# Optimization experiments

Measured on AMD Instinct MI355X. Metric: run time of the kernel, lower is better.

The kernel has to match this reference:

```python
import jax, jax.numpy as jnp
import numpy as np

B, T, K, V, D, C = 16, 16, 4, 10003, 256, 64  # batch, traj_len, beam, lid_size+3, dim_embed_loc, dim_com


def setup_inputs() -> dict:
    key = jax.random.key(0)
    ks = jax.random.split(key, 9)
    return {
        "loc_tar": jax.random.randint(ks[0], (B, T), 0, V),
        "zs": jax.random.normal(ks[1], (B, D), jnp.float32),
        "zt": jax.random.normal(ks[2], (B, D), jnp.float32),
        "E": jax.random.normal(ks[3], (V, D), jnp.float32) * 0.02,    # loc embedding table
        "W_v": jax.random.normal(ks[4], (D, V), jnp.float32) * 0.02,  # decoder output proj
        "b_v": jnp.zeros((V,), jnp.float32),
        "W_c": jax.random.normal(ks[5], (D, C), jnp.float32) * 0.05,  # LocCompressor
        "b_c": jnp.zeros((C,), jnp.float32),
        "W_t": jax.random.normal(ks[6], (C,), jnp.float32) * 0.05,    # temporal decoder
        "W_zt": jax.random.normal(ks[7], (D,), jnp.float32) * 0.05,
    }


def _decode(loc_tar, zs, E, W_v, b_v):
    # Beam-search decode faithful to the torch inference branch:
    # per-step full-seq decoder fwd, log_softmax, topk, (log-prob) product,
    # descending sort over M*K candidates, gather top 2K chains.
    chain_r = loc_tar.at[:, 1:].set(0)   # [B,T]; keep BOS, zero rest
    zs_r = zs                            # [B,D]
    prob = None
    for i in range(T - 1):
        emb = E[chain_r]                                     # [N,T,D] gather
        h = emb + zs_r[:, None, :]
        logp = jax.nn.log_softmax(h @ W_v + b_v, axis=-1)    # [N,T,V]
        p_i, idx_i = jax.lax.top_k(logp[:, i, :], K)         # [N,K]
        if i == 0:
            chain_r = jnp.repeat(chain_r, K, axis=0).at[:, 1].set(idx_i.reshape(-1))  # [B*K,T]
            prob = p_i                                       # [B,K]
            zs_r = jnp.repeat(zs_r, K, axis=0)
        else:
            M = chain_r.shape[0] // B                        # K at i=1, 2K after
            # NOTE: original multiplies log-probs (faithful to source)
            prob2 = (prob[:, :, None] * p_i.reshape(B, M, K)).reshape(B, M * K)
            order = jnp.argsort(-prob2, axis=-1)             # descending sort
            prob = jnp.take_along_axis(prob2, order, axis=-1)[:, :2 * K]
            ch = jnp.repeat(chain_r, K, axis=0).at[:, i + 1].set(idx_i.reshape(-1))
            ch = ch.reshape(B, M * K, T)
            chain_r = ch[jnp.arange(B)[:, None], order[:, :2 * K]].reshape(-1, T)  # [B*2K,T]
            zs_r = jnp.repeat(zs, 2 * K, axis=0)
    return chain_r.reshape(B, -1, T)[:, 0, 1:-1]             # best beam, [B,T-2]


def reference(loc_tar, zs, zt, E, W_v, b_v, W_c, b_c, W_t, W_zt):
    loc_chain = _decode(loc_tar, zs, E, W_v, b_v)            # [B,T-2] int
    loc_info = jnp.tanh(E[loc_chain] @ W_c + b_c)            # LocCompressor, [B,T-2,C]
    tim_chain = loc_info @ W_t + (zt @ W_zt)[:, None]        # temporal decoder, [B,T-2]
    return loc_chain, tim_chain
```

## Files before the change

### kernel.cpp

```cpp
#include <hip/hip_runtime.h>
#include <math.h>

#define BB 16
#define TT 16
#define KK 4
#define VV 10003
#define DD 256
#define CC 64
#define RPB 4
#define VT  1280
#define NVT 8
#define VP 10016
#define FNEG (-1e30f)

typedef float f32x4 __attribute__((ext_vector_type(4)));
typedef float f32x4u __attribute__((ext_vector_type(4), aligned(4)));

struct L4 { float v0, v1, v2, v3; int i0, i1, i2, i3; };

__device__ __forceinline__ void l4_init(L4 &l) {
  l.v0 = l.v1 = l.v2 = l.v3 = FNEG;
  l.i0 = l.i1 = l.i2 = l.i3 = 0x7fffffff;
}
__device__ __forceinline__ bool better(float v, int ix, float v2, int ix2) {
  return (v > v2) || (v == v2 && ix < ix2);
}
__device__ __forceinline__ void l4_insert(L4 &l, float v, int ix) {
  const bool c0 = better(v, ix, l.v0, l.i0);
  const bool c1 = better(v, ix, l.v1, l.i1);
  const bool c2 = better(v, ix, l.v2, l.i2);
  const bool c3 = better(v, ix, l.v3, l.i3);
  l.v3 = c3 ? (c2 ? l.v2 : v) : l.v3;  l.i3 = c3 ? (c2 ? l.i2 : ix) : l.i3;
  l.v2 = c2 ? (c1 ? l.v1 : v) : l.v2;  l.i2 = c2 ? (c1 ? l.i1 : ix) : l.i2;
  l.v1 = c1 ? (c0 ? l.v0 : v) : l.v1;  l.i1 = c1 ? (c0 ? l.i0 : ix) : l.i1;
  l.v0 = c0 ? v : l.v0;                l.i0 = c0 ? ix : l.i0;
}
__device__ __forceinline__ void l4_merge(L4 &a, const L4 &b) {
  l4_insert(a, b.v0, b.i0);
  l4_insert(a, b.v1, b.i1);
  l4_insert(a, b.v2, b.i2);
  l4_insert(a, b.v3, b.i3);
}
__device__ __forceinline__ L4 l4_shfl_xor(const L4 &a, int off) {
  L4 o;
  o.v0 = __shfl_xor(a.v0, off); o.i0 = __shfl_xor(a.i0, off);
  o.v1 = __shfl_xor(a.v1, off); o.i1 = __shfl_xor(a.i1, off);
  o.v2 = __shfl_xor(a.v2, off); o.i2 = __shfl_xor(a.i2, off);
  o.v3 = __shfl_xor(a.v3, off); o.i3 = __shfl_xor(a.i3, off);
  return o;
}

__global__ __launch_bounds__(256, 1)
void k_gemm(const float* __restrict__ E, const float* __restrict__ zs,
            const float* __restrict__ Wv, const float* __restrict__ bv,
            const int* __restrict__ loc_tar,
            const float* __restrict__ topP, const int* __restrict__ topI,
            const float* __restrict__ probIn, const int* __restrict__ chainIn,
            float* __restrict__ probOut, int* __restrict__ chainOut,
            float* __restrict__ Lg, int step, int N, int Mshift) {
  __shared__ __align__(16) float xs[RPB * DD];
  __shared__ int cs[RPB];
  __shared__ int selSrc[BB][8];
  __shared__ int selTok[BB][8];
  __shared__ float prS[BB * 8];

  const int t = threadIdx.x;
  const int tile = blockIdx.x % NVT;
  const int n0 = (blockIdx.x / NVT) * RPB;
  const int v0 = tile * VT;

  const int v4 = v0 + (t << 2);
  const int v1 = v0 + 1024 + t;
  const int v1ok = (v1 < VV);
  const int v1c = v1ok ? v1 : (VV - 1);

  if (step >= 2) {
    const int M = (step == 2) ? 4 : 8;
    const int nc = M * 4;
    const int c = t & 31;
    const int bh = t >> 5;
    for (int h = 0; h < 2; ++h) {
      const int b = bh + h * 8;
      float act;
      if (c < nc) {
        int mi = c >> 2, k = c & 3;
        act = probIn[b * 8 + mi] * topP[(b * M + mi) * 4 + k];
      } else {
        act = -INFINITY;
      }
      for (int j = 0; j < 8; ++j) {
        float rv = act; int ri = c;
#pragma unroll
        for (int off = 1; off < 32; off <<= 1) {
          float v2 = __shfl_xor(rv, off, 32);
          int   i2 = __shfl_xor(ri, off, 32);
          if (v2 > rv || (v2 == rv && i2 < ri)) { rv = v2; ri = i2; }
        }
        if (c == ri) act = -INFINITY;
        if (c == 0) {
          int mi = ri >> 2, k = ri & 3;
          int src = b * M + mi;
          int tok = topI[src * 4 + k]; if ((unsigned)tok >= VV) tok = 0;
          selSrc[b][j] = src;
          selTok[b][j] = tok;
          prS[b * 8 + j] = rv;
        }
      }
    }
    __syncthreads();
  }

  if (t < RPB) {
    int n = n0 + t;
    int ctok;
    if (step == 0)      ctok = loc_tar[n * TT];
    else if (step == 1) ctok = topI[(n >> 2) * 4 + (n & 3)];
    else                ctok = selTok[n >> 3][n & 7];
    if ((unsigned)ctok >= VV) ctok = 0;
    cs[t] = ctok;
  }
  __syncthreads();

  if (blockIdx.x == 0 && step >= 1) {
    if (step == 1) {
      for (int e = t; e < BB * KK * TT; e += 256) {
        int dst = e >> 4, q = e & 15;
        int bb = dst >> 2, kk = dst & 3;
        int val;
        if (q == 1) { int tok = topI[bb * 4 + kk]; if ((unsigned)tok >= VV) tok = 0; val = tok; }
        else if (q == 0) val = loc_tar[bb * TT];
        else val = 0;
        chainOut[dst * TT + q] = val;
      }
      if (t < BB * KK) {
        int bb = t >> 2, kk = t & 3;
        probOut[bb * 8 + kk] = topP[bb * 4 + kk];
      }
    } else {
      for (int e = t; e < BB * 8 * TT; e += 256) {
        int dst = e >> 4, q = e & 15;
        int bb = dst >> 3, j = dst & 7;
        int src = selSrc[bb][j];
        int val = (q == step) ? selTok[bb][j] : chainIn[src * TT + q];
        chainOut[dst * TT + q] = val;
      }
      if (t < BB * 8) probOut[t] = prS[t];
    }
  }

  for (int e = t; e < RPB * DD; e += 256) {
    int r = e >> 8, d = e & 255;
    int n = n0 + r;
    int b = n >> Mshift;
    xs[e] = E[cs[r] * DD + d] + zs[b * DD + d];
  }
  __syncthreads();

  const float* w4p = Wv + v4;
  const float* w1p = Wv + v1c;

  float acc4[RPB][4];
  float acc1[RPB];
#pragma unroll
  for (int r = 0; r < RPB; ++r) {
    acc1[r] = 0.f;
#pragma unroll
    for (int j = 0; j < 4; ++j) acc4[r][j] = 0.f;
  }

  f32x4u w4A[8], w4B[8];
  float  w1A[8], w1B[8];
  f32x4  h0A[RPB], h1A[RPB], h0B[RPB], h1B[RPB];

#pragma unroll
  for (int u = 0; u < 8; ++u) {
    w4A[u] = *(const f32x4u*)(w4p + (size_t)u * VV);
    w1A[u] = w1p[(size_t)u * VV];
  }
#pragma unroll
  for (int r = 0; r < RPB; ++r) {
    h0A[r] = *(const f32x4*)(xs + r * DD);
    h1A[r] = *(const f32x4*)(xs + r * DD + 4);
  }

  for (int d0 = 0; d0 < DD; d0 += 16) {
    const int dB = d0 + 8;
#pragma unroll
    for (int u = 0; u < 8; ++u) {
      w4B[u] = *(const f32x4u*)(w4p + (size_t)(dB + u) * VV);
      w1B[u] = w1p[(size_t)(dB + u) * VV];
    }
#pragma unroll
    for (int r = 0; r < RPB; ++r) {
      h0B[r] = *(const f32x4*)(xs + r * DD + dB);
      h1B[r] = *(const f32x4*)(xs + r * DD + dB + 4);
    }

#pragma unroll
    for (int u = 0; u < 8; ++u) {
#pragma unroll
      for (int r = 0; r < RPB; ++r) {
        const float hv = (u < 4) ? h0A[r][u] : h1A[r][u - 4];
#pragma unroll
        for (int j = 0; j < 4; ++j) acc4[r][j] = fmaf(hv, w4A[u][j], acc4[r][j]);
        acc1[r] = fmaf(hv, w1A[u], acc1[r]);
      }
    }

    const int dA = (d0 + 16 < DD) ? (d0 + 16) : 0;
#pragma unroll
    for (int u = 0; u < 8; ++u) {
      w4A[u] = *(const f32x4u*)(w4p + (size_t)(dA + u) * VV);
      w1A[u] = w1p[(size_t)(dA + u) * VV];
    }
#pragma unroll
    for (int r = 0; r < RPB; ++r) {
      h0A[r] = *(const f32x4*)(xs + r * DD + dA);
      h1A[r] = *(const f32x4*)(xs + r * DD + dA + 4);
    }

#pragma unroll
    for (int u = 0; u < 8; ++u) {
#pragma unroll
      for (int r = 0; r < RPB; ++r) {
        const float hv = (u < 4) ? h0B[r][u] : h1B[r][u - 4];
#pragma unroll
        for (int j = 0; j < 4; ++j) acc4[r][j] = fmaf(hv, w4B[u][j], acc4[r][j]);
        acc1[r] = fmaf(hv, w1B[u], acc1[r]);
      }
    }
  }

  const f32x4u bv4 = *(const f32x4u*)(bv + v4);
#pragma unroll
  for (int r = 0; r < RPB; ++r) {
    f32x4 o;
#pragma unroll
    for (int j = 0; j < 4; ++j) o[j] = acc4[r][j] + bv4[j];
    *(f32x4*)(Lg + (size_t)(n0 + r) * VP + v4) = o;
  }
  if (v1ok) {
    const float bvv = bv[v1];
#pragma unroll
    for (int r = 0; r < RPB; ++r)
      Lg[(size_t)(n0 + r) * VP + v1] = acc1[r] + bvv;
  }
}

__global__ __launch_bounds__(1024)
void k_red(const float* __restrict__ Lg, float* __restrict__ topP,
           int* __restrict__ topI) {
  __shared__ __align__(16) float row[VV];
  __shared__ float wmax[16];
  __shared__ float wv4[16 * 4];
  __shared__ int   wi4[16 * 4];
  __shared__ float leafS[128];

  const int n = blockIdx.x;
  const int t = threadIdx.x;
  const int lane = t & 63;
  const int wid = t >> 6;
  const float* grow = Lg + (size_t)n * VP;

  const int va = t << 2;
  const int vb = 4096 + (t << 2);
  const int vc = 8192 + (t << 2);
  f32x4 xa = *(const f32x4*)(grow + va);
  f32x4 xb = *(const f32x4*)(grow + vb);
  f32x4 xc;
  const bool cfull = (vc + 3 < VV);
  if (cfull) {
    xc = *(const f32x4*)(grow + vc);
  } else {
#pragma unroll
    for (int j = 0; j < 4; ++j) xc[j] = (vc + j < VV) ? grow[vc + j] : FNEG;
  }

  float m = FNEG;
  L4 top; l4_init(top);
#pragma unroll
  for (int j = 0; j < 4; ++j) { float x = xa[j]; if (x > m) m = x; l4_insert(top, x, va + j); }
#pragma unroll
  for (int j = 0; j < 4; ++j) { float x = xb[j]; if (x > m) m = x; l4_insert(top, x, vb + j); }
#pragma unroll
  for (int j = 0; j < 4; ++j) {
    if (vc + j < VV) { float x = xc[j]; if (x > m) m = x; l4_insert(top, x, vc + j); }
  }

  for (int off = 32; off; off >>= 1) {
    float m2 = __shfl_xor(m, off);
    if (m2 > m) m = m2;
    L4 o = l4_shfl_xor(top, off);
    l4_merge(top, o);
  }
  if (lane == 0) {
    wmax[wid] = m;
    wv4[wid * 4 + 0] = top.v0; wi4[wid * 4 + 0] = top.i0;
    wv4[wid * 4 + 1] = top.v1; wi4[wid * 4 + 1] = top.i1;
    wv4[wid * 4 + 2] = top.v2; wi4[wid * 4 + 2] = top.i2;
    wv4[wid * 4 + 3] = top.v3; wi4[wid * 4 + 3] = top.i3;
  }
  __syncthreads();

  float mm = wmax[lane & 15];
#pragma unroll
  for (int off = 8; off; off >>= 1) {
    float m2 = __shfl_xor(mm, off);
    if (m2 > mm) mm = m2;
  }
  const float gm = mm;

  L4 aa; l4_init(aa);
  if (wid == 0) {
    const int g = lane & 15;
    aa.v0 = wv4[g * 4 + 0]; aa.i0 = wi4[g * 4 + 0];
    aa.v1 = wv4[g * 4 + 1]; aa.i1 = wi4[g * 4 + 1];
    aa.v2 = wv4[g * 4 + 2]; aa.i2 = wi4[g * 4 + 2];
    aa.v3 = wv4[g * 4 + 3]; aa.i3 = wi4[g * 4 + 3];
#pragma unroll
    for (int off = 8; off; off >>= 1) {
      L4 o = l4_shfl_xor(aa, off);
      l4_merge(aa, o);
    }
  }

  {
    f32x4 ea, eb;
#pragma unroll
    for (int j = 0; j < 4; ++j) ea[j] = (float)exp((double)(xa[j] - gm));
#pragma unroll
    for (int j = 0; j < 4; ++j) eb[j] = (float)exp((double)(xb[j] - gm));
    *(f32x4*)(row + va) = ea;
    *(f32x4*)(row + vb) = eb;
    if (cfull) {
      f32x4 ec;
#pragma unroll
      for (int j = 0; j < 4; ++j) ec[j] = (float)exp((double)(xc[j] - gm));
      *(f32x4*)(row + vc) = ec;
    } else {
#pragma unroll
      for (int j = 0; j < 4; ++j)
        if (vc + j < VV) row[vc + j] = (float)exp((double)(xc[j] - gm));
    }
  }
  __syncthreads();

  {
    const int g = t >> 3, j = t & 7;
    int base = 0, nn = VV;
#pragma unroll
    for (int k = 6; k >= 0; --k) {
      int half = nn >> 1;
      int n2 = half - (half & 7);
      if ((g >> k) & 1) { base += n2; nn -= n2; } else nn = n2;
    }
    const float* a = row + base;
    const int full = nn & ~7;
    float r = a[j];
    for (int i = 8 + j; i < full; i += 8) r += a[i];
    float s = r + __shfl_xor(r, 1);
    s = s + __shfl_xor(s, 2);
    s = s + __shfl_xor(s, 4);
    if (j == 0) {
      for (int i = full; i < nn; ++i) s += a[i];
      leafS[g] = s;
    }
  }
  __syncthreads();

  if (t < 64) {
    float v = leafS[2 * t] + leafS[2 * t + 1];
#pragma unroll
    for (int l = 0; l < 6; ++l) {
      float x0 = __shfl(v, t * 2);
      float x1 = __shfl(v, t * 2 + 1);
      v = x0 + x1;
    }
    if (t == 0) {
      float ls = (float)log((double)v);
      topP[n * 4 + 0] = (aa.v0 - gm) - ls;  topI[n * 4 + 0] = aa.i0;
      topP[n * 4 + 1] = (aa.v1 - gm) - ls;  topI[n * 4 + 1] = aa.i1;
      topP[n * 4 + 2] = (aa.v2 - gm) - ls;  topI[n * 4 + 2] = aa.i2;
      topP[n * 4 + 3] = (aa.v3 - gm) - ls;  topI[n * 4 + 3] = aa.i3;
    }
  }
}

__global__ __launch_bounds__(64)
void k_final(const int* __restrict__ chainIn, const float* __restrict__ probIn,
             const float* __restrict__ topP, const int* __restrict__ topI,
             const float* __restrict__ E,
             const float* __restrict__ Wc, const float* __restrict__ bc,
             const float* __restrict__ Wt, const float* __restrict__ zt,
             const float* __restrict__ Wzt, float* __restrict__ out) {
  int blk = blockIdx.x;
  int b = blk / (TT - 2), tpos = blk % (TT - 2);
  int lane = threadIdx.x;

  const int c = lane & 31;
  int mi = c >> 2, k = c & 3;
  float act = probIn[b * 8 + mi] * topP[(b * 8 + mi) * 4 + k];
  float rv = act; int ri = c;
#pragma unroll
  for (int off = 1; off < 32; off <<= 1) {
    float v2 = __shfl_xor(rv, off, 32);
    int   i2 = __shfl_xor(ri, off, 32);
    if (v2 > rv || (v2 == rv && i2 < ri)) { rv = v2; ri = i2; }
  }
  const int src = b * 8 + (ri >> 2);
  int loc = chainIn[src * TT + 1 + tpos];
  if ((unsigned)loc >= VV) loc = 0;

  double acc = (double)bc[lane];
  const float* er = E + loc * DD;
  for (int d = 0; d < DD; ++d) acc += (double)er[d] * (double)Wc[d * CC + lane];
  double val = tanh(acc) * (double)Wt[lane];
  const float* ztr = zt + b * DD;
#pragma unroll
  for (int q = 0; q < 4; ++q) val += (double)ztr[lane * 4 + q] * (double)Wzt[lane * 4 + q];
  for (int off = 32; off; off >>= 1) val += __shfl_down(val, off);
  if (lane == 0) {
    out[b * (TT - 2) + tpos] = (float)loc;
    out[BB * (TT - 2) + b * (TT - 2) + tpos] = (float)val;
  }
}

extern "C" void kernel_launch(void* const* d_in, const int* in_sizes, int n_in,
                              void* d_out, int out_size, void* d_ws, size_t ws_size,
                              hipStream_t stream) {
  const int*   loc_tar = (const int*)  d_in[0];
  const float* zs      = (const float*)d_in[1];
  const float* zt      = (const float*)d_in[2];
  const float* E       = (const float*)d_in[3];
  const float* Wv      = (const float*)d_in[4];
  const float* bv      = (const float*)d_in[5];
  const float* Wc      = (const float*)d_in[6];
  const float* bc      = (const float*)d_in[7];
  const float* Wt      = (const float*)d_in[8];
  const float* Wzt     = (const float*)d_in[9];
  float* out = (float*)d_out;

  char* w = (char*)d_ws;
  float* Lg     = (float*)(w);
  float* topP   = (float*)(w + 5128192);
  int*   topI   = (int*)  (w + 5130240);
  float* probA  = (float*)(w + 5132288);
  float* probB  = (float*)(w + 5132800);
  int*   chainA = (int*)  (w + 5133312);
  int*   chainB = (int*)  (w + 5141504);

  float* pIn = probA; float* pOut = probB;
  int*   cIn = chainA; int*  cOut = chainB;

  k_gemm<<<(16 / RPB) * NVT, 256, 0, stream>>>(E, zs, Wv, bv, loc_tar,
      topP, topI, pIn, cIn, pOut, cOut, Lg, 0, 16, 0);
  k_red<<<16, 1024, 0, stream>>>(Lg, topP, topI);

  for (int i = 1; i < TT - 1; ++i) {
    int N = (i == 1) ? (BB * KK) : (BB * 2 * KK);
    int Mshift = (i == 1) ? 2 : 3;
    k_gemm<<<(N / RPB) * NVT, 256, 0, stream>>>(E, zs, Wv, bv, loc_tar,
        topP, topI, pIn, cIn, pOut, cOut, Lg, i, N, Mshift);
    k_red<<<N, 1024, 0, stream>>>(Lg, topP, topI);
    float* pt = pIn; pIn = pOut; pOut = pt;
    int*   ct = cIn; cIn = cOut; cOut = ct;
  }

  k_final<<<BB * (TT - 2), 64, 0, stream>>>(cIn, pIn, topP, topI,
                                            E, Wc, bc, Wt, zt, Wzt, out);
}
```

Baseline: 1.019 ms.

## Split vocab tiles finer, emit per-tile max from GEMM, split softmax reduction in halves

The GEMM now uses 16 vocab tiles of 640 columns with 2-wide vector loads and asks for two blocks per CU. Each block also writes per-row tile maxima, so the reduction kernel no longer computes the global max itself. The log-softmax/top-k reduction is split across two blocks per row, and a new small combine kernel merges the partial sums and top-4 lists. This raises parallelism at small batch sizes but adds one kernel launch per step and uses narrower loads per thread.

```diff
diff --git a/kernel.cpp b/kernel.cpp
--- a/kernel.cpp
+++ b/kernel.cpp
@@ -8,13 +8,15 @@
 #define DD 256
 #define CC 64
 #define RPB 4
-#define VT  1280
-#define NVT 8
+#define VT  640
+#define NVT 16
 #define VP 10016
 #define FNEG (-1e30f)
+#define NSPL 5000
 
 typedef float f32x4 __attribute__((ext_vector_type(4)));
 typedef float f32x4u __attribute__((ext_vector_type(4), aligned(4)));
+typedef float f32x2u __attribute__((ext_vector_type(2), aligned(4)));
 
 struct L4 { float v0, v1, v2, v3; int i0, i1, i2, i3; };
 
@@ -50,29 +52,34 @@
   return o;
 }
 
-__global__ __launch_bounds__(256, 1)
+__global__ __launch_bounds__(256, 2)
 void k_gemm(const float* __restrict__ E, const float* __restrict__ zs,
             const float* __restrict__ Wv, const float* __restrict__ bv,
             const int* __restrict__ loc_tar,
             const float* __restrict__ topP, const int* __restrict__ topI,
             const float* __restrict__ probIn, const int* __restrict__ chainIn,
             float* __restrict__ probOut, int* __restrict__ chainOut,
-            float* __restrict__ Lg, int step, int N, int Mshift) {
+            float* __restrict__ Lg, float* __restrict__ Gmax,
+            int step, int N, int Mshift) {
   __shared__ __align__(16) float xs[RPB * DD];
   __shared__ int cs[RPB];
   __shared__ int selSrc[BB][8];
   __shared__ int selTok[BB][8];
   __shared__ float prS[BB * 8];
+  __shared__ float wmx[4][RPB];
 
   const int t = threadIdx.x;
   const int tile = blockIdx.x % NVT;
   const int n0 = (blockIdx.x / NVT) * RPB;
   const int v0 = tile * VT;
 
-  const int v4 = v0 + (t << 2);
-  const int v1 = v0 + 1024 + t;
-  const int v1ok = (v1 < VV);
-  const int v1c = v1ok ? v1 : (VV - 1);
+  const int vp = v0 + (t << 1);
+  const int vpok = (vp + 1 < VV);
+  const int vpc = vpok ? vp : 0;
+  int ve = v0 + 512 + t;
+  int veok = (t < 128) && (ve < VV);
+  if (v0 + 512 >= VV && t == 0) { ve = VV - 1; veok = 1; }
+  const int vec = veok ? ve : (VV - 1);
 
   if (step >= 2) {
     const int M = (step == 2) ? 4 : 8;
@@ -156,25 +163,24 @@
   }
   __syncthreads();
 
-  const float* w4p = Wv + v4;
-  const float* w1p = Wv + v1c;
-
-  float acc4[RPB][4];
+  const float* w2p = Wv + vpc;
+  const float* w1p = Wv + vec;
+
+  float acc2[RPB][2];
   float acc1[RPB];
 #pragma unroll
   for (int r = 0; r < RPB; ++r) {
     acc1[r] = 0.f;
-#pragma unroll
-    for (int j = 0; j < 4; ++j) acc4[r][j] = 0.f;
-  }
-
-  f32x4u w4A[8], w4B[8];
+    acc2[r][0] = 0.f; acc2[r][1] = 0.f;
+  }
+
+  f32x2u w2A[8], w2B[8];
   float  w1A[8], w1B[8];
   f32x4  h0A[RPB], h1A[RPB], h0B[RPB], h1B[RPB];
 
 #pragma unroll
   for (int u = 0; u < 8; ++u) {
-    w4A[u] = *(const f32x4u*)(w4p + (size_t)u * VV);
+    w2A[u] = *(const f32x2u*)(w2p + (size_t)u * VV);
     w1A[u] = w1p[(size_t)u * VV];
   }
 #pragma unroll
@@ -187,7 +193,7 @@
     const int dB = d0 + 8;
 #pragma unroll
     for (int u = 0; u < 8; ++u) {
-      w4B[u] = *(const f32x4u*)(w4p + (size_t)(dB + u) * VV);
+      w2B[u] = *(const f32x2u*)(w2p + (size_t)(dB + u) * VV);
       w1B[u] = w1p[(size_t)(dB + u) * VV];
     }
 #pragma unroll
@@ -201,16 +207,16 @@
 #pragma unroll
       for (int r = 0; r < RPB; ++r) {
         const float hv = (u < 4) ? h0A[r][u] : h1A[r][u - 4];
-#pragma unroll
-        for (int j = 0; j < 4; ++j) acc4[r][j] = fmaf(hv, w4A[u][j], acc4[r][j]);
-        acc1[r] = fmaf(hv, w1A[u], acc1[r]);
+        acc2[r][0] = fmaf(hv, w2A[u][0], acc2[r][0]);
+        acc2[r][1] = fmaf(hv, w2A[u][1], acc2[r][1]);
+        acc1[r]    = fmaf(hv, w1A[u],    acc1[r]);
       }
     }
 
     const int dA = (d0 + 16 < DD) ? (d0 + 16) : 0;
 #pragma unroll
     for (int u = 0; u < 8; ++u) {
-      w4A[u] = *(const f32x4u*)(w4p + (size_t)(dA + u) * VV);
+      w2A[u] = *(const f32x2u*)(w2p + (size_t)(dA + u) * VV);
       w1A[u] = w1p[(size_t)(dA + u) * VV];
     }
 #pragma unroll
@@ -224,91 +230,108 @@
 #pragma unroll
       for (int r = 0; r < RPB; ++r) {
         const float hv = (u < 4) ? h0B[r][u] : h1B[r][u - 4];
-#pragma unroll
-        for (int j = 0; j < 4; ++j) acc4[r][j] = fmaf(hv, w4B[u][j], acc4[r][j]);
-        acc1[r] = fmaf(hv, w1B[u], acc1[r]);
-      }
-    }
-  }
-
-  const f32x4u bv4 = *(const f32x4u*)(bv + v4);
+        acc2[r][0] = fmaf(hv, w2B[u][0], acc2[r][0]);
+        acc2[r][1] = fmaf(hv, w2B[u][1], acc2[r][1]);
+        acc1[r]    = fmaf(hv, w1B[u],    acc1[r]);
+      }
+    }
+  }
+
+  f32x2u b2; b2[0] = 0.f; b2[1] = 0.f;
+  if (vpok) b2 = *(const f32x2u*)(bv + vp);
+  const float be = veok ? bv[ve] : 0.f;
+
+  float mr[RPB];
 #pragma unroll
   for (int r = 0; r < RPB; ++r) {
-    f32x4 o;
-#pragma unroll
-    for (int j = 0; j < 4; ++j) o[j] = acc4[r][j] + bv4[j];
-    *(f32x4*)(Lg + (size_t)(n0 + r) * VP + v4) = o;
-  }
-  if (v1ok) {
-    const float bvv = bv[v1];
-#pragma unroll
-    for (int r = 0; r < RPB; ++r)
-      Lg[(size_t)(n0 + r) * VP + v1] = acc1[r] + bvv;
+    const float o0 = acc2[r][0] + b2[0];
+    const float o1 = acc2[r][1] + b2[1];
+    const float oe = acc1[r] + be;
+    if (vpok) {
+      f32x2u o; o[0] = o0; o[1] = o1;
+      *(f32x2u*)(Lg + (size_t)(n0 + r) * VP + vp) = o;
+    }
+    if (veok) Lg[(size_t)(n0 + r) * VP + ve] = oe;
+    float m = FNEG;
+    if (vpok) m = fmaxf(o0, o1);
+    if (veok) m = fmaxf(m, oe);
+    mr[r] = m;
+  }
+#pragma unroll
+  for (int off = 32; off; off >>= 1) {
+#pragma unroll
+    for (int r = 0; r < RPB; ++r) mr[r] = fmaxf(mr[r], __shfl_xor(mr[r], off));
+  }
+  if ((t & 63) == 0) {
+#pragma unroll
+    for (int r = 0; r < RPB; ++r) wmx[t >> 6][r] = mr[r];
+  }
+  __syncthreads();
+  if (t < RPB) {
+    float m = fmaxf(fmaxf(wmx[0][t], wmx[1][t]), fmaxf(wmx[2][t], wmx[3][t]));
+    Gmax[(n0 + t) * NVT + tile] = m;
   }
 }
 
 __global__ __launch_bounds__(1024)
-void k_red(const float* __restrict__ Lg, float* __restrict__ topP,
-           int* __restrict__ topI) {
-  __shared__ __align__(16) float row[VV];
-  __shared__ float wmax[16];
+void k_red(const float* __restrict__ Lg, const float* __restrict__ Gmax,
+           float* __restrict__ recS, float* __restrict__ recV,
+           int* __restrict__ recI) {
+  __shared__ __align__(16) float rowh[5003];
   __shared__ float wv4[16 * 4];
   __shared__ int   wi4[16 * 4];
-  __shared__ float leafS[128];
-
-  const int n = blockIdx.x;
+  __shared__ float leafS[64];
+
+  const int blk = blockIdx.x;
+  const int n = blk >> 1, half = blk & 1;
   const int t = threadIdx.x;
   const int lane = t & 63;
   const int wid = t >> 6;
   const float* grow = Lg + (size_t)n * VP;
 
-  const int va = t << 2;
-  const int vb = 4096 + (t << 2);
-  const int vc = 8192 + (t << 2);
-  f32x4 xa = *(const f32x4*)(grow + va);
-  f32x4 xb = *(const f32x4*)(grow + vb);
-  f32x4 xc;
-  const bool cfull = (vc + 3 < VV);
-  if (cfull) {
-    xc = *(const f32x4*)(grow + vc);
-  } else {
-#pragma unroll
-    for (int j = 0; j < 4; ++j) xc[j] = (vc + j < VV) ? grow[vc + j] : FNEG;
-  }
-
-  float m = FNEG;
+  const int base0 = half ? NSPL : 0;
+  const int lim   = half ? VV : NSPL;
+
+  float gm = Gmax[n * NVT + 0];
+#pragma unroll
+  for (int i = 1; i < NVT; ++i) gm = fmaxf(gm, Gmax[n * NVT + i]);
+
+  const int v1 = base0 + (t << 2);
+  f32x4 xa = *(const f32x4*)(grow + v1);
+  const int v2 = base0 + 4096 + (t << 2);
+  const bool p2 = (v2 < lim);
+  const bool p2full = (v2 + 3 < lim);
+  f32x4 xb;
+#pragma unroll
+  for (int j = 0; j < 4; ++j) xb[j] = FNEG;
+  if (p2) {
+    if (p2full) xb = *(const f32x4*)(grow + v2);
+    else {
+#pragma unroll
+      for (int j = 0; j < 4; ++j) if (v2 + j < lim) xb[j] = grow[v2 + j];
+    }
+  }
+
   L4 top; l4_init(top);
 #pragma unroll
-  for (int j = 0; j < 4; ++j) { float x = xa[j]; if (x > m) m = x; l4_insert(top, x, va + j); }
-#pragma unroll
-  for (int j = 0; j < 4; ++j) { float x = xb[j]; if (x > m) m = x; l4_insert(top, x, vb + j); }
-#pragma unroll
-  for (int j = 0; j < 4; ++j) {
-    if (vc + j < VV) { float x = xc[j]; if (x > m) m = x; l4_insert(top, x, vc + j); }
+  for (int j = 0; j < 4; ++j) l4_insert(top, xa[j], v1 + j);
+  if (p2) {
+#pragma unroll
+    for (int j = 0; j < 4; ++j)
+      if (v2 + j < lim) l4_insert(top, xb[j], v2 + j);
   }
 
   for (int off = 32; off; off >>= 1) {
-    float m2 = __shfl_xor(m, off);
-    if (m2 > m) m = m2;
     L4 o = l4_shfl_xor(top, off);
     l4_merge(top, o);
   }
   if (lane == 0) {
-    wmax[wid] = m;
     wv4[wid * 4 + 0] = top.v0; wi4[wid * 4 + 0] = top.i0;
     wv4[wid * 4 + 1] = top.v1; wi4[wid * 4 + 1] = top.i1;
     wv4[wid * 4 + 2] = top.v2; wi4[wid * 4 + 2] = top.i2;
     wv4[wid * 4 + 3] = top.v3; wi4[wid * 4 + 3] = top.i3;
   }
   __syncthreads();
-
-  float mm = wmax[lane & 15];
-#pragma unroll
-  for (int off = 8; off; off >>= 1) {
-    float m2 = __shfl_xor(mm, off);
-    if (m2 > mm) mm = m2;
-  }
-  const float gm = mm;
 
   L4 aa; l4_init(aa);
   if (wid == 0) {
@@ -325,36 +348,35 @@
   }
 
   {
-    f32x4 ea, eb;
+    f32x4 ea;
 #pragma unroll
     for (int j = 0; j < 4; ++j) ea[j] = (float)exp((double)(xa[j] - gm));
-#pragma unroll
-    for (int j = 0; j < 4; ++j) eb[j] = (float)exp((double)(xb[j] - gm));
-    *(f32x4*)(row + va) = ea;
-    *(f32x4*)(row + vb) = eb;
-    if (cfull) {
-      f32x4 ec;
-#pragma unroll
-      for (int j = 0; j < 4; ++j) ec[j] = (float)exp((double)(xc[j] - gm));
-      *(f32x4*)(row + vc) = ec;
-    } else {
-#pragma unroll
-      for (int j = 0; j < 4; ++j)
-        if (vc + j < VV) row[vc + j] = (float)exp((double)(xc[j] - gm));
+    *(f32x4*)(rowh + (v1 - base0)) = ea;
+    if (p2) {
+      if (p2full) {
+        f32x4 eb;
+#pragma unroll
+        for (int j = 0; j < 4; ++j) eb[j] = (float)exp((double)(xb[j] - gm));
+        *(f32x4*)(rowh + (v2 - base0)) = eb;
+      } else {
+#pragma unroll
+        for (int j = 0; j < 4; ++j)
+          if (v2 + j < lim) rowh[v2 - base0 + j] = (float)exp((double)(xb[j] - gm));
+      }
     }
   }
   __syncthreads();
 
-  {
+  if (t < 512) {
     const int g = t >> 3, j = t & 7;
-    int base = 0, nn = VV;
-#pragma unroll
-    for (int k = 6; k >= 0; --k) {
-      int half = nn >> 1;
-      int n2 = half - (half & 7);
-      if ((g >> k) & 1) { base += n2; nn -= n2; } else nn = n2;
-    }
-    const float* a = row + base;
+    int bs = base0, nn = lim - base0;
+#pragma unroll
+    for (int k = 5; k >= 0; --k) {
+      int hh = nn >> 1;
+      int n2 = hh - (hh & 7);
+      if ((g >> k) & 1) { bs += n2; nn -= n2; } else nn = n2;
+    }
+    const float* a = rowh + (bs - base0);
     const int full = nn & ~7;
     float r = a[j];
     for (int i = 8 + j; i < full; i += 8) r += a[i];
@@ -368,22 +390,42 @@
   }
   __syncthreads();
 
-  if (t < 64) {
+  if (t < 32) {
     float v = leafS[2 * t] + leafS[2 * t + 1];
 #pragma unroll
-    for (int l = 0; l < 6; ++l) {
+    for (int l = 0; l < 5; ++l) {
       float x0 = __shfl(v, t * 2);
       float x1 = __shfl(v, t * 2 + 1);
       v = x0 + x1;
     }
     if (t == 0) {
-      float ls = (float)log((double)v);
-      topP[n * 4 + 0] = (aa.v0 - gm) - ls;  topI[n * 4 + 0] = aa.i0;
-      topP[n * 4 + 1] = (aa.v1 - gm) - ls;  topI[n * 4 + 1] = aa.i1;
-      topP[n * 4 + 2] = (aa.v2 - gm) - ls;  topI[n * 4 + 2] = aa.i2;
-      topP[n * 4 + 3] = (aa.v3 - gm) - ls;  topI[n * 4 + 3] = aa.i3;
-    }
-  }
+      recS[n * 2 + half] = v;
+      recV[n * 8 + half * 4 + 0] = aa.v0;  recI[n * 8 + half * 4 + 0] = aa.i0;
+      recV[n * 8 + half * 4 + 1] = aa.v1;  recI[n * 8 + half * 4 + 1] = aa.i1;
+      recV[n * 8 + half * 4 + 2] = aa.v2;  recI[n * 8 + half * 4 + 2] = aa.i2;
+      recV[n * 8 + half * 4 + 3] = aa.v3;  recI[n * 8 + half * 4 + 3] = aa.i3;
+    }
+  }
+}
+
+__global__ __launch_bounds__(128)
+void k_comb(const float* __restrict__ Gmax, const float* __restrict__ recS,
+            const float* __restrict__ recV, const int* __restrict__ recI,
+            float* __restrict__ topP, int* __restrict__ topI, int N) {
+  const int n = threadIdx.x;
+  if (n >= N) return;
+  float gm = Gmax[n * NVT + 0];
+#pragma unroll
+  for (int i = 1; i < NVT; ++i) gm = fmaxf(gm, Gmax[n * NVT + i]);
+  L4 a; l4_init(a);
+#pragma unroll
+  for (int j = 0; j < 8; ++j) l4_insert(a, recV[n * 8 + j], recI[n * 8 + j]);
+  const float s = recS[n * 2 + 0] + recS[n * 2 + 1];
+  const float ls = (float)log((double)s);
+  topP[n * 4 + 0] = (a.v0 - gm) - ls;  topI[n * 4 + 0] = a.i0;
+  topP[n * 4 + 1] = (a.v1 - gm) - ls;  topI[n * 4 + 1] = a.i1;
+  topP[n * 4 + 2] = (a.v2 - gm) - ls;  topI[n * 4 + 2] = a.i2;
+  topP[n * 4 + 3] = (a.v3 - gm) - ls;  topI[n * 4 + 3] = a.i3;
 }
 
 __global__ __launch_bounds__(64)
@@ -448,20 +490,26 @@
   float* probB  = (float*)(w + 5132800);
   int*   chainA = (int*)  (w + 5133312);
   int*   chainB = (int*)  (w + 5141504);
+  float* Gmax   = (float*)(w + 5149696);
+  float* recS   = (float*)(w + 5157888);
+  float* recV   = (float*)(w + 5158912);
+  int*   recI   = (int*)  (w + 5163008);
 
   float* pIn = probA; float* pOut = probB;
   int*   cIn = chainA; int*  cOut = chainB;
 
   k_gemm<<<(16 / RPB) * NVT, 256, 0, stream>>>(E, zs, Wv, bv, loc_tar,
-      topP, topI, pIn, cIn, pOut, cOut, Lg, 0, 16, 0);
-  k_red<<<16, 1024, 0, stream>>>(Lg, topP, topI);
+      topP, topI, pIn, cIn, pOut, cOut, Lg, Gmax, 0, 16, 0);
+  k_red<<<16 * 2, 1024, 0, stream>>>(Lg, Gmax, recS, recV, recI);
+  k_comb<<<1, 128, 0, stream>>>(Gmax, recS, recV, recI, topP, topI, 16);
 
   for (int i = 1; i < TT - 1; ++i) {
     int N = (i == 1) ? (BB * KK) : (BB * 2 * KK);
     int Mshift = (i == 1) ? 2 : 3;
     k_gemm<<<(N / RPB) * NVT, 256, 0, stream>>>(E, zs, Wv, bv, loc_tar,
-        topP, topI, pIn, cIn, pOut, cOut, Lg, i, N, Mshift);
-    k_red<<<N, 1024, 0, stream>>>(Lg, topP, topI);
+        topP, topI, pIn, cIn, pOut, cOut, Lg, Gmax, i, N, Mshift);
+    k_red<<<N * 2, 1024, 0, stream>>>(Lg, Gmax, recS, recV, recI);
+    k_comb<<<1, 128, 0, stream>>>(Gmax, recS, recV, recI, topP, topI, N);
     float* pt = pIn; pIn = pOut; pOut = pt;
     int*   ct = cIn; cIn = cOut; cOut = ct;
   }
```

New measurement: 1.330 ms. 1.31x slower.
